# Optimization experiments

Hardware: AMD Instinct MI355X
Metric: run time of the kernel (lower is better)

## Reference

```python
import jax, jax.numpy as jnp
import numpy as np

N = 50000   # nodes
E = 800000  # edges
D = 64      # feature dim
C = 1.0     # curvature
MIN_NORM = 1e-15
BALL_EPS = 4e-3  # float32 projection epsilon (hgcn convention)


def _artanh(x):
    x = jnp.clip(x, -1.0 + 1e-7, 1.0 - 1e-7)
    return jnp.arctanh(x)


def _norm(x):
    return jnp.maximum(jnp.linalg.norm(x, axis=-1, keepdims=True), MIN_NORM)


def expmap0(u, c):
    # euclidean2poincare: tangent at origin -> ball
    sqrt_c = jnp.sqrt(c)
    u_norm = _norm(u)
    return jnp.tanh(sqrt_c * u_norm) * u / (sqrt_c * u_norm)


def logmap0(p, c):
    # poincare2euclidean: ball -> tangent at origin
    sqrt_c = jnp.sqrt(c)
    p_norm = _norm(p)
    return _artanh(sqrt_c * p_norm) * p / (sqrt_c * p_norm)


def proj(x, c):
    sqrt_c = jnp.sqrt(c)
    norm = _norm(x)
    maxnorm = (1.0 - BALL_EPS) / sqrt_c
    return jnp.where(norm > maxnorm, x / norm * maxnorm, x)


def mobius_matvec(m, x, c):
    # m: [out, in], x: [N, in]
    sqrt_c = jnp.sqrt(c)
    x_norm = _norm(x)                      # [N,1]
    mx = x @ m.T                           # [N,out]
    mx_norm = _norm(mx)                    # [N,1]
    res = jnp.tanh(mx_norm / x_norm * _artanh(sqrt_c * x_norm)) * mx / (mx_norm * sqrt_c)
    zero_mask = jnp.all(mx == 0.0, axis=-1, keepdims=True)
    return jnp.where(zero_mask, jnp.zeros_like(res), res)


def setup_inputs() -> dict:
    key = jax.random.key(0)
    k1, k2, k3, k4 = jax.random.split(key, 4)
    # node features: small norm so points lie well inside the unit ball
    x = jax.random.normal(k1, (N, D), dtype=jnp.float32) * 0.05
    # xavier_uniform-ish scale for the weight
    W = jax.random.normal(k2, (D, D), dtype=jnp.float32) * np.float32(np.sqrt(2.0 / D))
    edge_index = jax.random.randint(k3, (2, E), 0, N)
    edge_weight = jax.random.uniform(k4, (E,), dtype=jnp.float32)
    return {"x": x, "W": W, "edge_weight": edge_weight, "edge_index": edge_index}


def reference(x, W, edge_weight, edge_index):
    c = jnp.float32(C)
    # Linear (dropout=0, no bias): mobius matvec in the ball
    hidden = mobius_matvec(W, x, c)                       # [N,D] in ball
    # poincare2euclidean
    hidden_e = logmap0(hidden, c)                         # [N,D]
    # sparse adjacency aggregation: support = A @ hidden_e
    row, col = edge_index[0], edge_index[1]
    msgs = edge_weight[:, None] * hidden_e[col]           # [E,D]
    support = jax.ops.segment_sum(msgs, row, num_segments=N)  # [N,D]
    # euclidean2poincare
    support = expmap0(support, c)
    # HypAct: logmap0(c_in) -> relu -> expmap0(c_out) -> proj
    xt = jax.nn.relu(logmap0(support, c))
    out = proj(expmap0(xt, c), c)
    return out
```

## Files before the change

kernel.cpp:

```cpp
#include <hip/hip_runtime.h>
#include <hip/hip_bf16.h>
#include <math.h>

#define DD 64
#define BROWS 64
#define BSH 6
#define MAXB 1024
#define CAPB 1536
#define BINB 1024
#define BINC 6144
typedef unsigned long long u64;
typedef unsigned int u32;
typedef unsigned short u16;

__global__ __launch_bounds__(1024) void hgcn_zero0(int* __restrict__ bcur,
                                                   int* __restrict__ nspill) {
  const int i = threadIdx.x;
  if (i < MAXB) bcur[i] = 0;
  if (i == 0) nspill[0] = 0;
}

__global__ __launch_bounds__(1024) void hgcn_linbin(const float* __restrict__ x,
                                                    const float* __restrict__ W,
                                                    __hip_bfloat16* __restrict__ he,
                                                    const int* __restrict__ ei,
                                                    const float* __restrict__ ew,
                                                    int* __restrict__ bcur,
                                                    u64* __restrict__ stage,
                                                    u64* __restrict__ spill,
                                                    int* __restrict__ nspill,
                                                    int n, int ne, int nbin) {
  const int tid = threadIdx.x;
  if ((int)blockIdx.x < nbin) {
    __shared__ int h[MAXB], cur[MAXB], gp[MAXB];
    h[tid] = 0; cur[tid] = 0;
    __syncthreads();
    const int eb = blockIdx.x * BINC;
    const int m = min(BINC, ne - eb);
    for (int i = tid; i < m; i += BINB) atomicAdd(&h[ei[eb + i] >> BSH], 1);
    __syncthreads();
    gp[tid] = h[tid] ? atomicAdd(&bcur[tid], h[tid]) : 0;
    __syncthreads();
    for (int i = tid; i < m; i += BINB) {
      const int r = ei[eb + i];
      const int c = ei[ne + eb + i];
      const float w = ew[eb + i];
      const int b = r >> BSH;
      const int pos = gp[b] + atomicAdd(&cur[b], 1);
      if (pos < CAPB) {
        stage[(size_t)b * CAPB + pos] =
            ((u64)__float_as_uint(w) << 32) | ((u32)(r & (BROWS - 1)) << 16) | (u32)c;
      } else {
        const int sp = atomicAdd(nspill, 1);
        spill[sp] = ((u64)__float_as_uint(w) << 32) | ((u32)(r & 0xffff) << 16) | (u32)c;
      }
    }
  } else {
    __shared__ float Wl[64][68];
    __shared__ float xs[64][64];
    const int lb = blockIdx.x - nbin;
    for (int i = tid; i < 64 * 64; i += 1024) Wl[i >> 6][i & 63] = W[i];
    const int wave = tid >> 6, lane = tid & 63;
    const int rbase = lb * 64 + wave * 4;
    float xv[4];
    #pragma unroll
    for (int q = 0; q < 4; ++q) {
      const int row = rbase + q;
      xv[q] = (row < n) ? x[(size_t)row * DD + lane] : 0.f;
      xs[wave * 4 + q][lane] = xv[q];
    }
    __syncthreads();
    const int j0 = (lane >> 3) & 7;
    #pragma unroll
    for (int q = 0; q < 4; ++q) {
      const int row = rbase + q;
      if (row >= n) break;
      float nx2 = xv[q] * xv[q];
      #pragma unroll
      for (int m = 1; m < 64; m <<= 1) nx2 += __shfl_xor(nx2, m);
      const float nx = fmaxf(sqrtf(nx2), 1e-15f);
      const float s  = atanhf(fminf(nx, 1.f - 1e-7f)) / nx;
      float acc = 0.f;
      #pragma unroll
      for (int jj = 0; jj < 16; ++jj) {
        const int k = ((jj + j0) & 15) << 2;
        const float4 xk = *reinterpret_cast<const float4*>(&xs[wave * 4 + q][k]);
        const float4 wk = *reinterpret_cast<const float4*>(&Wl[lane][k]);
        acc = fmaf(xk.x, wk.x, acc);
        acc = fmaf(xk.y, wk.y, acc);
        acc = fmaf(xk.z, wk.z, acc);
        acc = fmaf(xk.w, wk.w, acc);
      }
      he[(size_t)row * DD + lane] = __float2bfloat16(acc * s);
    }
  }
}

__global__ __launch_bounds__(1024) void hgcn_bagg(const u16* __restrict__ he,
                                                  const u64* __restrict__ stage,
                                                  const int* __restrict__ bcur,
                                                  const u64* __restrict__ spill,
                                                  const int* __restrict__ nspill,
                                                  float* __restrict__ out, int n) {
  __shared__ u64 edr[CAPB];
  __shared__ u64 ed[CAPB];
  __shared__ int lh[BROWS + 1];
  __shared__ int lcur[BROWS];
  const int t = threadIdx.x;
  const int b = blockIdx.x;
  const u64* sb = stage + (size_t)b * CAPB;
  const int cnt = min(bcur[b], CAPB);

  for (int i = t; i < cnt; i += 1024) edr[i] = sb[i];
  if (t < BROWS) lcur[t] = 0;
  __syncthreads();
  for (int i = t; i < cnt; i += 1024)
    atomicAdd(&lcur[(int)((edr[i] >> 16) & (BROWS - 1))], 1);
  __syncthreads();
  if (t < 64) {
    const int v = lcur[t];
    int sc = v;
    #pragma unroll
    for (int d = 1; d < 64; d <<= 1) {
      const int u2 = __shfl_up(sc, d);
      if (t >= d) sc += u2;
    }
    lh[t] = sc - v;
    lcur[t] = sc - v;
    if (t == 63) lh[64] = sc;
  }
  __syncthreads();
  for (int i = t; i < cnt; i += 1024) {
    const u64 p = edr[i];
    const int rl = (int)((p >> 16) & (BROWS - 1));
    const int pos = atomicAdd(&lcur[rl], 1);
    ed[pos] = p;
  }
  __syncthreads();

  const int row = t >> 4;
  const int u = t & 15;
  const int s = u >> 3;
  const int l = u & 7;
  float a[8] = {0.f, 0.f, 0.f, 0.f, 0.f, 0.f, 0.f, 0.f};

  int j = lh[row] + s;
  const int je = lh[row + 1];
  uint4 q = {0, 0, 0, 0};
  float w = 0.f;
  if (j < je) {
    const u64 p = ed[j];
    w = __uint_as_float((u32)(p >> 32));
    q = reinterpret_cast<const uint4*>(he + ((size_t)(p & 0xffffu) << 6))[l];
  }
  while (j < je) {
    const uint4 qc = q;
    const float wc = w;
    const int jn = j + 2;
    if (jn < je) {
      const u64 p = ed[jn];
      w = __uint_as_float((u32)(p >> 32));
      q = reinterpret_cast<const uint4*>(he + ((size_t)(p & 0xffffu) << 6))[l];
    }
    a[0] = fmaf(wc, __uint_as_float(qc.x << 16), a[0]);
    a[1] = fmaf(wc, __uint_as_float(qc.x & 0xffff0000u), a[1]);
    a[2] = fmaf(wc, __uint_as_float(qc.y << 16), a[2]);
    a[3] = fmaf(wc, __uint_as_float(qc.y & 0xffff0000u), a[3]);
    a[4] = fmaf(wc, __uint_as_float(qc.z << 16), a[4]);
    a[5] = fmaf(wc, __uint_as_float(qc.z & 0xffff0000u), a[5]);
    a[6] = fmaf(wc, __uint_as_float(qc.w << 16), a[6]);
    a[7] = fmaf(wc, __uint_as_float(qc.w & 0xffff0000u), a[7]);
    j = jn;
  }

  const int ns = nspill[0];
  for (int sidx = 0; sidx < ns; ++sidx) {
    const u64 p = spill[sidx];
    const int grow = (int)((p >> 16) & 0xffffu);
    if ((grow >> BSH) != b) continue;
    if ((grow & (BROWS - 1)) != row || s != 0) continue;
    const float ww = __uint_as_float((u32)(p >> 32));
    const uint4 qq = reinterpret_cast<const uint4*>(he + ((size_t)(p & 0xffffu) << 6))[l];
    a[0] = fmaf(ww, __uint_as_float(qq.x << 16), a[0]);
    a[1] = fmaf(ww, __uint_as_float(qq.x & 0xffff0000u), a[1]);
    a[2] = fmaf(ww, __uint_as_float(qq.y << 16), a[2]);
    a[3] = fmaf(ww, __uint_as_float(qq.y & 0xffff0000u), a[3]);
    a[4] = fmaf(ww, __uint_as_float(qq.z << 16), a[4]);
    a[5] = fmaf(ww, __uint_as_float(qq.z & 0xffff0000u), a[5]);
    a[6] = fmaf(ww, __uint_as_float(qq.w << 16), a[6]);
    a[7] = fmaf(ww, __uint_as_float(qq.w & 0xffff0000u), a[7]);
  }

  #pragma unroll
  for (int k = 0; k < 8; ++k) a[k] += __shfl_xor(a[k], 8);

  float ss = 0.f;
  #pragma unroll
  for (int k = 0; k < 8; ++k) { a[k] = fmaxf(a[k], 0.f); ss = fmaf(a[k], a[k], ss); }
  ss += __shfl_xor(ss, 1); ss += __shfl_xor(ss, 2); ss += __shfl_xor(ss, 4);
  const float nu = fmaxf(sqrtf(ss), 1e-15f);
  const float th = tanhf(nu);
  const float maxn = 1.0f - 4e-3f;
  const float scale = (th > maxn) ? (maxn / nu) : (th / nu);
  const int grow = (b << BSH) + row;
  if (s == 0 && grow < n) {
    float4* op = reinterpret_cast<float4*>(out + (size_t)grow * DD + (size_t)l * 8);
    op[0] = float4{a[0] * scale, a[1] * scale, a[2] * scale, a[3] * scale};
    op[1] = float4{a[4] * scale, a[5] * scale, a[6] * scale, a[7] * scale};
  }
}

__global__ __launch_bounds__(256) void hgcn_linf32(const float* __restrict__ x,
                                                   const float* __restrict__ W,
                                                   float* __restrict__ he, int n) {
  __shared__ float Wl[64][68];
  __shared__ float xs[4][64];
  const int tid = threadIdx.x;
  for (int i = tid; i < 64 * 64; i += 256) Wl[i >> 6][i & 63] = W[i];
  const int wave = tid >> 6, lane = tid & 63;
  const int row = blockIdx.x * 4 + wave;
  float xv = 0.f;
  if (row < n) xv = x[row * DD + lane];
  xs[wave][lane] = xv;
  __syncthreads();
  if (row >= n) return;
  float nx2 = xv * xv;
  #pragma unroll
  for (int m = 1; m < 64; m <<= 1) nx2 += __shfl_xor(nx2, m);
  const float nx = fmaxf(sqrtf(nx2), 1e-15f);
  const float s = atanhf(fminf(nx, 1.f - 1e-7f)) / nx;
  const int j0 = (lane >> 3) & 7;
  float acc = 0.f;
  #pragma unroll
  for (int jj = 0; jj < 16; ++jj) {
    const int k = ((jj + j0) & 15) << 2;
    const float4 xk = *reinterpret_cast<const float4*>(&xs[wave][k]);
    const float4 wk = *reinterpret_cast<const float4*>(&Wl[lane][k]);
    acc = fmaf(xk.x, wk.x, acc); acc = fmaf(xk.y, wk.y, acc);
    acc = fmaf(xk.z, wk.z, acc); acc = fmaf(xk.w, wk.w, acc);
  }
  he[row * DD + lane] = acc * s;
}

__global__ __launch_bounds__(256) void hgcn_zero(float* __restrict__ p, int n4) {
  const int i = blockIdx.x * 256 + threadIdx.x;
  if (i < n4) reinterpret_cast<float4*>(p)[i] = float4{0.f, 0.f, 0.f, 0.f};
}

__global__ __launch_bounds__(256) void hgcn_scatter(const float* __restrict__ he,
                                                    const int* __restrict__ ei,
                                                    const float* __restrict__ ew,
                                                    float* __restrict__ sup, int ne) {
  const int t = blockIdx.x * 256 + threadIdx.x;
  const int e = t >> 4, l = t & 15;
  if (e >= ne) return;
  const int row = ei[e];
  const int col = ei[ne + e];
  const float w = ew[e];
  const float4 v = *reinterpret_cast<const float4*>(he + (size_t)col * DD + l * 4);
  float* dst = sup + (size_t)row * DD + l * 4;
  unsafeAtomicAdd(dst + 0, w * v.x);
  unsafeAtomicAdd(dst + 1, w * v.y);
  unsafeAtomicAdd(dst + 2, w * v.z);
  unsafeAtomicAdd(dst + 3, w * v.w);
}

__global__ __launch_bounds__(256) void hgcn_final(const float* __restrict__ sup,
                                                  float* __restrict__ out, int n) {
  const int t = blockIdx.x * 256 + threadIdx.x;
  const int r = t >> 4, l = t & 15;
  if (r >= n) return;
  float4 v = *reinterpret_cast<const float4*>(sup + (size_t)r * DD + l * 4);
  v.x = fmaxf(v.x, 0.f); v.y = fmaxf(v.y, 0.f);
  v.z = fmaxf(v.z, 0.f); v.w = fmaxf(v.w, 0.f);
  float p = v.x*v.x + v.y*v.y + v.z*v.z + v.w*v.w;
  p += __shfl_xor(p, 1); p += __shfl_xor(p, 2);
  p += __shfl_xor(p, 4); p += __shfl_xor(p, 8);
  const float nu = fmaxf(sqrtf(p), 1e-15f);
  const float th = tanhf(nu);
  float scale = th / nu;
  const float maxn = 1.0f - 4e-3f;
  if (th > maxn) scale = maxn / nu;
  float4 o = {v.x*scale, v.y*scale, v.z*scale, v.w*scale};
  *reinterpret_cast<float4*>(out + (size_t)r * DD + l * 4) = o;
}

extern "C" void kernel_launch(void* const* d_in, const int* in_sizes, int n_in,
                              void* d_out, int out_size, void* d_ws, size_t ws_size,
                              hipStream_t stream) {
  const float* x  = (const float*)d_in[0];
  const float* W  = (const float*)d_in[1];
  const float* ew = (const float*)d_in[2];
  const int*   ei = (const int*)d_in[3];
  const int n  = in_sizes[0] / DD;
  const int ne = in_sizes[2];
  const int nb = (n + BROWS - 1) / BROWS;

  size_t off_he    = 0;
  size_t off_stage = off_he + (((size_t)n * DD * 2 + 15) / 16) * 16;
  size_t off_spill = off_stage + (size_t)MAXB * CAPB * 8;
  size_t off_bcur  = off_spill + (size_t)ne * 8;
  size_t off_nsp   = off_bcur + MAXB * 4;
  size_t need      = off_nsp + 64;

  const size_t mean = (size_t)ne / (size_t)nb;
  size_t sig = 1;
  while (sig * sig < mean) ++sig;
  const bool capOK = mean + 8 * sig <= CAPB;

  if (ws_size >= need && n <= 65535 && nb <= MAXB && capOK) {
    __hip_bfloat16* he = (__hip_bfloat16*)((char*)d_ws + off_he);
    u64* stage  = (u64*)((char*)d_ws + off_stage);
    u64* spill  = (u64*)((char*)d_ws + off_spill);
    int* bcur   = (int*)((char*)d_ws + off_bcur);
    int* nspill = (int*)((char*)d_ws + off_nsp);
    float* out  = (float*)d_out;

    const int nbin = (ne + BINC - 1) / BINC;
    const int nlin = (n + 63) / 64;

    hipLaunchKernelGGL(hgcn_zero0,  dim3(1),           dim3(1024), 0, stream, bcur, nspill);
    hipLaunchKernelGGL(hgcn_linbin, dim3(nbin + nlin), dim3(1024), 0, stream,
                       x, W, he, ei, ew, bcur, stage, spill, nspill, n, ne, nbin);
    hipLaunchKernelGGL(hgcn_bagg,   dim3(nb),          dim3(1024), 0, stream,
                       (const u16*)he, stage, bcur, spill, nspill, out, n);
  } else {
    float* he  = (float*)d_out;
    float* sup = (float*)d_ws;
    float* out = (float*)d_out;
    const int n4 = n * DD / 4;
    hipLaunchKernelGGL(hgcn_zero,    dim3((n4 + 255) / 256),       dim3(256), 0, stream, sup, n4);
    hipLaunchKernelGGL(hgcn_linf32,  dim3((n + 3) / 4),            dim3(256), 0, stream, x, W, he, n);
    hipLaunchKernelGGL(hgcn_scatter, dim3((ne * 16 + 255) / 256),  dim3(256), 0, stream, he, ei, ew, sup, ne);
    hipLaunchKernelGGL(hgcn_final,   dim3((n * 16 + 255) / 256),   dim3(256), 0, stream, sup, out, n);
  }
}
```

Measured before the change: 68.07 us.

## Cache edge data in registers for binning and use fp16 dot2 matvec

The binning branch now loads each edge's row, column and weight once into registers. It takes each edge's slot rank from the histogram atomic itself, which removes the second global read pass and the second shared-memory atomic pass. Blocks shrink to 512 threads with 3072 edges each. The linear branch keeps W in registers as packed fp16 and uses fdot2 over 128 rows per block, with a fast log-based artanh. This drops the shared W tile but lowers matvec precision to fp16 inputs and adds per-row wave synchronisation through shared memory with no barrier.

```diff
diff --git a/kernel.cpp b/kernel.cpp
--- a/kernel.cpp
+++ b/kernel.cpp
@@ -7,11 +7,13 @@
 #define BSH 6
 #define MAXB 1024
 #define CAPB 1536
-#define BINB 1024
-#define BINC 6144
+#define BINB 512
+#define BINC 3072
+#define LROWS 128
 typedef unsigned long long u64;
 typedef unsigned int u32;
 typedef unsigned short u16;
+typedef __fp16 f16x2 __attribute__((ext_vector_type(2)));
 
 __global__ __launch_bounds__(1024) void hgcn_zero0(int* __restrict__ bcur,
                                                    int* __restrict__ nspill) {
@@ -20,77 +22,84 @@
   if (i == 0) nspill[0] = 0;
 }
 
-__global__ __launch_bounds__(1024) void hgcn_linbin(const float* __restrict__ x,
-                                                    const float* __restrict__ W,
-                                                    __hip_bfloat16* __restrict__ he,
-                                                    const int* __restrict__ ei,
-                                                    const float* __restrict__ ew,
-                                                    int* __restrict__ bcur,
-                                                    u64* __restrict__ stage,
-                                                    u64* __restrict__ spill,
-                                                    int* __restrict__ nspill,
-                                                    int n, int ne, int nbin) {
+__global__ __launch_bounds__(512) void hgcn_linbin(const float* __restrict__ x,
+                                                   const float* __restrict__ W,
+                                                   __hip_bfloat16* __restrict__ he,
+                                                   const int* __restrict__ ei,
+                                                   const float* __restrict__ ew,
+                                                   int* __restrict__ bcur,
+                                                   u64* __restrict__ stage,
+                                                   u64* __restrict__ spill,
+                                                   int* __restrict__ nspill,
+                                                   int n, int ne, int nbin) {
   const int tid = threadIdx.x;
   if ((int)blockIdx.x < nbin) {
-    __shared__ int h[MAXB], cur[MAXB], gp[MAXB];
-    h[tid] = 0; cur[tid] = 0;
+    __shared__ int h[MAXB], gp[MAXB];
+    h[tid] = 0; h[tid + 512] = 0;
     __syncthreads();
     const int eb = blockIdx.x * BINC;
     const int m = min(BINC, ne - eb);
-    for (int i = tid; i < m; i += BINB) atomicAdd(&h[ei[eb + i] >> BSH], 1);
+    int r[6], c[6], rk[6];
+    float w[6];
+    int cnt = 0;
+    #pragma unroll
+    for (int k = 0; k < 6; ++k) {
+      const int i = tid + k * BINB;
+      if (i < m) {
+        r[k] = ei[eb + i];
+        c[k] = ei[ne + eb + i];
+        w[k] = ew[eb + i];
+        rk[k] = atomicAdd(&h[r[k] >> BSH], 1);
+        cnt = k + 1;
+      }
+    }
     __syncthreads();
-    gp[tid] = h[tid] ? atomicAdd(&bcur[tid], h[tid]) : 0;
+    {
+      const int v0 = h[tid];
+      gp[tid] = v0 ? atomicAdd(&bcur[tid], v0) : 0;
+      const int v1 = h[tid + 512];
+      gp[tid + 512] = v1 ? atomicAdd(&bcur[tid + 512], v1) : 0;
+    }
     __syncthreads();
-    for (int i = tid; i < m; i += BINB) {
-      const int r = ei[eb + i];
-      const int c = ei[ne + eb + i];
-      const float w = ew[eb + i];
-      const int b = r >> BSH;
-      const int pos = gp[b] + atomicAdd(&cur[b], 1);
+    for (int k = 0; k < cnt; ++k) {
+      const int b = r[k] >> BSH;
+      const int pos = gp[b] + rk[k];
       if (pos < CAPB) {
         stage[(size_t)b * CAPB + pos] =
-            ((u64)__float_as_uint(w) << 32) | ((u32)(r & (BROWS - 1)) << 16) | (u32)c;
+            ((u64)__float_as_uint(w[k]) << 32) | ((u32)(r[k] & (BROWS - 1)) << 16) | (u32)c[k];
       } else {
         const int sp = atomicAdd(nspill, 1);
-        spill[sp] = ((u64)__float_as_uint(w) << 32) | ((u32)(r & 0xffff) << 16) | (u32)c;
+        spill[sp] = ((u64)__float_as_uint(w[k]) << 32) | ((u32)(r[k] & 0xffff) << 16) | (u32)c[k];
       }
     }
   } else {
-    __shared__ float Wl[64][68];
-    __shared__ float xs[64][64];
-    const int lb = blockIdx.x - nbin;
-    for (int i = tid; i < 64 * 64; i += 1024) Wl[i >> 6][i & 63] = W[i];
+    __shared__ f16x2 xsh[8][32];
+    const int lb = (int)blockIdx.x - nbin;
     const int wave = tid >> 6, lane = tid & 63;
-    const int rbase = lb * 64 + wave * 4;
-    float xv[4];
+    f16x2 Wh[32];
     #pragma unroll
-    for (int q = 0; q < 4; ++q) {
-      const int row = rbase + q;
-      xv[q] = (row < n) ? x[(size_t)row * DD + lane] : 0.f;
-      xs[wave * 4 + q][lane] = xv[q];
-    }
-    __syncthreads();
-    const int j0 = (lane >> 3) & 7;
-    #pragma unroll
-    for (int q = 0; q < 4; ++q) {
+    for (int m4 = 0; m4 < 16; ++m4) {
+      const float4 wv = *reinterpret_cast<const float4*>(W + lane * 64 + m4 * 4);
+      Wh[2 * m4]     = __builtin_amdgcn_cvt_pkrtz(wv.x, wv.y);
+      Wh[2 * m4 + 1] = __builtin_amdgcn_cvt_pkrtz(wv.z, wv.w);
+    }
+    const int rbase = lb * LROWS + wave * 16;
+    for (int q = 0; q < 16; ++q) {
       const int row = rbase + q;
       if (row >= n) break;
-      float nx2 = xv[q] * xv[q];
+      const float xv = x[(size_t)row * DD + lane];
+      float nx2 = xv * xv;
       #pragma unroll
-      for (int m = 1; m < 64; m <<= 1) nx2 += __shfl_xor(nx2, m);
+      for (int mm = 1; mm < 64; mm <<= 1) nx2 += __shfl_xor(nx2, mm);
       const float nx = fmaxf(sqrtf(nx2), 1e-15f);
-      const float s  = atanhf(fminf(nx, 1.f - 1e-7f)) / nx;
+      const float z  = fminf(nx, 1.f - 1e-7f);
+      const float s  = 0.5f * __logf((1.f + z) / (1.f - z)) / nx;
+      const float xo = __shfl_xor(xv, 1);
+      if (!(lane & 1)) xsh[wave][lane >> 1] = __builtin_amdgcn_cvt_pkrtz(xv, xo);
       float acc = 0.f;
       #pragma unroll
-      for (int jj = 0; jj < 16; ++jj) {
-        const int k = ((jj + j0) & 15) << 2;
-        const float4 xk = *reinterpret_cast<const float4*>(&xs[wave * 4 + q][k]);
-        const float4 wk = *reinterpret_cast<const float4*>(&Wl[lane][k]);
-        acc = fmaf(xk.x, wk.x, acc);
-        acc = fmaf(xk.y, wk.y, acc);
-        acc = fmaf(xk.z, wk.z, acc);
-        acc = fmaf(xk.w, wk.w, acc);
-      }
+      for (int m2 = 0; m2 < 32; ++m2)
+        acc = __builtin_amdgcn_fdot2(xsh[wave][m2], Wh[m2], acc, false);
       he[(size_t)row * DD + lane] = __float2bfloat16(acc * s);
     }
   }
@@ -317,10 +326,10 @@
     float* out  = (float*)d_out;
 
     const int nbin = (ne + BINC - 1) / BINC;
-    const int nlin = (n + 63) / 64;
+    const int nlin = (n + LROWS - 1) / LROWS;
 
     hipLaunchKernelGGL(hgcn_zero0,  dim3(1),           dim3(1024), 0, stream, bcur, nspill);
-    hipLaunchKernelGGL(hgcn_linbin, dim3(nbin + nlin), dim3(1024), 0, stream,
+    hipLaunchKernelGGL(hgcn_linbin, dim3(nbin + nlin), dim3(512),  0, stream,
                        x, W, he, ei, ew, bcur, stage, spill, nspill, n, ne, nbin);
     hipLaunchKernelGGL(hgcn_bagg,   dim3(nb),          dim3(1024), 0, stream,
                        (const u16*)he, stage, bcur, spill, nspill, out, n);
```

Result: faster. 60.98 us (-10.4%).
